# Kernel optimization log

Hardware: AMD Instinct MI355X
Metric: run time of the kernel (lower is better)

The kernel has to match this reference:

```python
import jax, jax.numpy as jnp
import numpy as np
import math

B, L, E, H = 512, 200, 64, 4
D = E // H
NEG = jnp.float32(-(2.0 ** 32) + 1.0)


def setup_inputs() -> dict:
    key = jax.random.key(0)
    ks = jax.random.split(key, 12)
    inp = jax.random.normal(ks[0], (B, L, E), dtype=jnp.float32)
    # realistic variable-length histories: mask[b, t] = t < len_b, len_b in [1, L]
    lens = jax.random.randint(ks[1], (B, 1), 1, L + 1)
    mask = jnp.arange(L)[None, :] < lens  # [B, L] bool
    s = 1.0 / math.sqrt(E)
    pos_enc = jax.random.normal(ks[2], (1, L, E), dtype=jnp.float32)
    Wk = jax.random.uniform(ks[3], (E, E), jnp.float32, -s, s)
    bk = jnp.zeros((E,), jnp.float32)
    Wv = jax.random.uniform(ks[4], (E, E), jnp.float32, -s, s)
    bv = jnp.zeros((E,), jnp.float32)
    Wq = jax.random.uniform(ks[5], (E, E), jnp.float32, -s, s)
    bq = jnp.zeros((E,), jnp.float32)
    Wf = jax.random.uniform(ks[6], (E, E), jnp.float32, -s, s)
    bf = jnp.zeros((E,), jnp.float32)
    return {"input": inp, "mask": mask, "pos_enc": pos_enc,
            "Wk": Wk, "bk": bk, "Wv": Wv, "bv": bv,
            "Wq": Wq, "bq": bq, "Wf": Wf, "bf": bf}


def reference(input, mask, pos_enc, Wk, bk, Wv, bv, Wq, bq, Wf, bf):
    x = input + pos_enc  # [B, L, E]
    # project and split heads: [B, H, L, D]
    def split(t):
        return t.reshape(B, L, H, D).transpose(0, 2, 1, 3)
    k = split(x @ Wk.T + bk)
    v = split(x @ Wv.T + bv)
    q = split(x @ Wq.T + bq) / math.sqrt(D)
    scores = jnp.einsum('bhqd,bhkd->bhqk', q, k)  # [B, H, L, L]
    # key_mask in torch code broadcasts over dim 3 (mask on the QUERY axis),
    # query_mask is its transpose (mask on the KEY axis). Combined: both must be valid.
    both = mask[:, None, :, None] & mask[:, None, None, :]  # [B, 1, L, L]
    scores = jnp.where(both, scores, NEG)
    attn = jax.nn.softmax(scores, axis=-1)
    # dropout is identity at inference; omitted deterministically
    out = jnp.einsum('bhqk,bhkd->bhqd', attn, v)
    out = out.transpose(0, 2, 1, 3).reshape(B, L, E)
    out = out @ Wf.T + bf
    fm = mask.astype(jnp.float32)[:, :, None]  # [B, L, 1]
    lens = jnp.sum(fm, axis=1)  # [B, 1]
    pooled = jnp.sum(out * fm, axis=1) / (lens + 1e-8)  # [B, E]
    return pooled
```

## Files before the change

kernel.cpp:

```cpp
#include <hip/hip_runtime.h>
#include <hip/hip_fp16.h>
#include <math.h>

#define Bn 512
#define Ln 200
#define En 64
#define Hn 4
#define Dn 16
#define NT13 13
#define RMAX 208
#define XS 72
#define KS 36
#define VS 212

typedef _Float16 __f16;
typedef __f16 f16x4 __attribute__((ext_vector_type(4)));
typedef __f16 f16x8 __attribute__((ext_vector_type(8)));
typedef float f32x4 __attribute__((ext_vector_type(4)));

__device__ __forceinline__ f16x8 pack8(float4 a, float4 b) {
    f16x8 r;
    r[0] = (__f16)a.x; r[1] = (__f16)a.y; r[2] = (__f16)a.z; r[3] = (__f16)a.w;
    r[4] = (__f16)b.x; r[5] = (__f16)b.y; r[6] = (__f16)b.z; r[7] = (__f16)b.w;
    return r;
}

__global__ __launch_bounds__(256, 3) void fused_kernel(
    const float* __restrict__ input, const int* __restrict__ mask,
    const float* __restrict__ pos_enc,
    const float* __restrict__ Wk, const float* __restrict__ bk,
    const float* __restrict__ Wv, const float* __restrict__ bv,
    const float* __restrict__ Wq, const float* __restrict__ bq,
    float* __restrict__ pooled)
{
    __shared__ __align__(16) __f16 xw[4][16 * XS];
    __shared__ __align__(16) __f16 Kh[RMAX * KS];
    __shared__ __align__(16) __f16 Qh[RMAX * KS];
    __shared__ __align__(16) __f16 Vt[32 * VS];
    __shared__ float red[4][16];
    __shared__ int cnt_red[4];

    const int tid  = threadIdx.x;
    const int b    = blockIdx.x >> 1, hp = blockIdx.x & 1;
    const int wave = tid >> 6, lane = tid & 63;
    const int quad = lane >> 4, ln16 = lane & 15;

    const int mv = (tid < Ln) ? mask[b * Ln + tid] : 0;

    f16x8 bfr[3][2][2];
    #pragma unroll
    for (int m = 0; m < 3; ++m) {
        const float* W = (m == 0) ? Wk : (m == 1) ? Wv : Wq;
        #pragma unroll
        for (int ct = 0; ct < 2; ++ct)
            #pragma unroll
            for (int ks = 0; ks < 2; ++ks) {
                const float4* wp = (const float4*)(W + (size_t)(hp * 32 + ct * 16 + ln16) * 64) + (ks * 8 + quad * 2);
                bfr[m][ct][ks] = pack8(wp[0], wp[1]);
            }
    }
    float bkv[2], bvv[2], bqv[2];
    #pragma unroll
    for (int ct = 0; ct < 2; ++ct) {
        int cg = hp * 32 + ct * 16 + ln16;
        bkv[ct] = bk[cg]; bvv[ct] = bv[cg]; bqv[ct] = bq[cg];
    }

    const float4* in4 = (const float4*)(input + (size_t)b * Ln * En);
    const float4* pe4 = (const float4*)pos_enc;
    __f16* myx = xw[wave];

    for (int rt = wave; rt < NT13; rt += 4) {
        #pragma unroll
        for (int i = 0; i < 4; ++i) {
            const int gi = lane + (i << 6);
            const int r = gi >> 4, c4 = gi & 15;
            const int R = rt * 16 + r;
            float4 xv = {0,0,0,0}, pv = {0,0,0,0};
            if (R < Ln) { xv = in4[R * 16 + c4]; pv = pe4[R * 16 + c4]; }
            f16x4 hx;
            hx[0] = (__f16)(xv.x + pv.x); hx[1] = (__f16)(xv.y + pv.y);
            hx[2] = (__f16)(xv.z + pv.z); hx[3] = (__f16)(xv.w + pv.w);
            *(f16x4*)(myx + r * XS + c4 * 4) = hx;
        }

        f16x8 af[2];
        #pragma unroll
        for (int ks = 0; ks < 2; ++ks)
            af[ks] = *(const f16x8*)(myx + ln16 * XS + ks * 32 + quad * 8);

        f32x4 acc[3][2];
        #pragma unroll
        for (int m = 0; m < 3; ++m)
            #pragma unroll
            for (int ct = 0; ct < 2; ++ct)
                acc[m][ct] = (f32x4){0.f, 0.f, 0.f, 0.f};
        #pragma unroll
        for (int ks = 0; ks < 2; ++ks)
            #pragma unroll
            for (int m = 0; m < 3; ++m)
                #pragma unroll
                for (int ct = 0; ct < 2; ++ct)
                    acc[m][ct] = __builtin_amdgcn_mfma_f32_16x16x32_f16(af[ks], bfr[m][ct][ks], acc[m][ct], 0, 0, 0);

        #pragma unroll
        for (int ct = 0; ct < 2; ++ct) {
            #pragma unroll
            for (int j = 0; j < 4; ++j) {
                int t = rt * 16 + quad * 4 + j;
                Kh[t * KS + ct * 16 + ln16] = (__f16)(acc[0][ct][j] + bkv[ct]);
                Qh[t * KS + ct * 16 + ln16] = (__f16)((acc[2][ct][j] + bqv[ct]) * 0.25f);
            }
            f16x4 vp;
            #pragma unroll
            for (int j = 0; j < 4; ++j) vp[j] = (__f16)(acc[1][ct][j] + bvv[ct]);
            *(f16x4*)(Vt + (ct * 16 + ln16) * VS + rt * 16 + quad * 4) = vp;
        }
    }

    int c = (mv != 0) ? 1 : 0;
    #pragma unroll
    for (int off = 32; off; off >>= 1) c += __shfl_down(c, off, 64);
    if (lane == 0) cnt_red[wave] = c;
    __syncthreads();
    const int len = cnt_red[0] + cnt_red[1] + cnt_red[2] + cnt_red[3];
    const int nt  = (len + 15) >> 4;

    const int hl   = wave >> 1;
    const int hoff = hl * 16;
    const int npair = (nt + 1) >> 1;
    f32x4 pool = {0.f, 0.f, 0.f, 0.f};

    for (int p = (wave & 1); p < npair; p += 2) {
        const int qt0 = 2 * p, qt1 = 2 * p + 1;
        const int qr1 = min(qt1 * 16 + ln16, RMAX - 1);
        const f16x4 qf0 = *(const f16x4*)(Qh + (qt0 * 16 + ln16) * KS + hoff + quad * 4);
        const f16x4 qf1 = *(const f16x4*)(Qh + qr1 * KS + hoff + quad * 4);
        f32x4 o20 = {0,0,0,0}, o21 = {0,0,0,0};
        float l0 = 0.f, l1 = 0.f;

        for (int kt = 0; kt < nt - 1; ++kt) {
            const f16x4 kf = *(const f16x4*)(Kh + (kt * 16 + ln16) * KS + hoff + quad * 4);
            const f16x4 vf = *(const f16x4*)(Vt + (hoff + ln16) * VS + kt * 16 + quad * 4);
            f32x4 s0 = __builtin_amdgcn_mfma_f32_16x16x16f16(kf, qf0, (f32x4){0,0,0,0}, 0, 0, 0);
            f32x4 s1 = __builtin_amdgcn_mfma_f32_16x16x16f16(kf, qf1, (f32x4){0,0,0,0}, 0, 0, 0);
            f16x4 pf0, pf1;
            #pragma unroll
            for (int j = 0; j < 4; ++j) {
                float p0 = __expf(fminf(s0[j], 10.f));
                float p1 = __expf(fminf(s1[j], 10.f));
                l0 += p0; l1 += p1;
                pf0[j] = (__f16)p0; pf1[j] = (__f16)p1;
            }
            o20 = __builtin_amdgcn_mfma_f32_16x16x16f16(vf, pf0, o20, 0, 0, 0);
            o21 = __builtin_amdgcn_mfma_f32_16x16x16f16(vf, pf1, o21, 0, 0, 0);
        }
        {
            const int kt = nt - 1;
            const int kbase = kt * 16 + quad * 4;
            const f16x4 kf = *(const f16x4*)(Kh + (kt * 16 + ln16) * KS + hoff + quad * 4);
            const f16x4 vf = *(const f16x4*)(Vt + (hoff + ln16) * VS + kt * 16 + quad * 4);
            f32x4 s0 = __builtin_amdgcn_mfma_f32_16x16x16f16(kf, qf0, (f32x4){0,0,0,0}, 0, 0, 0);
            f32x4 s1 = __builtin_amdgcn_mfma_f32_16x16x16f16(kf, qf1, (f32x4){0,0,0,0}, 0, 0, 0);
            f16x4 pf0, pf1;
            #pragma unroll
            for (int j = 0; j < 4; ++j) {
                const bool kok = (kbase + j) < len;
                float p0 = kok ? __expf(fminf(s0[j], 10.f)) : 0.f;
                float p1 = kok ? __expf(fminf(s1[j], 10.f)) : 0.f;
                l0 += p0; l1 += p1;
                pf0[j] = (__f16)p0; pf1[j] = (__f16)p1;
            }
            o20 = __builtin_amdgcn_mfma_f32_16x16x16f16(vf, pf0, o20, 0, 0, 0);
            o21 = __builtin_amdgcn_mfma_f32_16x16x16f16(vf, pf1, o21, 0, 0, 0);
        }

        l0 += __shfl_xor(l0, 16, 64); l0 += __shfl_xor(l0, 32, 64);
        l1 += __shfl_xor(l1, 16, 64); l1 += __shfl_xor(l1, 32, 64);
        const float rs0 = (qt0 * 16 + ln16 < len) ? 1.f / l0 : 0.f;
        const float rs1 = (qt1 * 16 + ln16 < len) ? 1.f / l1 : 0.f;
        #pragma unroll
        for (int j = 0; j < 4; ++j)
            pool[j] = fmaf(o20[j], rs0, fmaf(o21[j], rs1, pool[j]));
    }

    #pragma unroll
    for (int j = 0; j < 4; ++j) {
        #pragma unroll
        for (int off = 1; off < 16; off <<= 1) pool[j] += __shfl_xor(pool[j], off, 64);
    }
    if (ln16 == 0) {
        #pragma unroll
        for (int j = 0; j < 4; ++j) red[wave][quad * 4 + j] = pool[j];
    }
    __syncthreads();
    if (tid < 32) {
        int hl2 = tid >> 4, vd = tid & 15;
        float sres = red[hl2 * 2][vd] + red[hl2 * 2 + 1][vd];
        pooled[b * En + hp * 32 + hl2 * 16 + vd] = sres / ((float)len + 1e-8f);
    }
}

__global__ __launch_bounds__(256) void final_kernel(
    const float* __restrict__ pooled, const float* __restrict__ Wf,
    const float* __restrict__ bf_, float* __restrict__ out)
{
    __shared__ float Wfs[En * 65];
    __shared__ float accs[4][En];
    const int tid = threadIdx.x, wave = tid >> 6, lane = tid & 63;
    const int b = blockIdx.x * 4 + wave;

    const float4* Wf4 = (const float4*)Wf;
    for (int idx4 = tid; idx4 < En * 16; idx4 += 256) {
        int e = idx4 >> 4, i4 = idx4 & 15;
        float4 w = Wf4[idx4];
        Wfs[e * 65 + i4 * 4 + 0] = w.x;
        Wfs[e * 65 + i4 * 4 + 1] = w.y;
        Wfs[e * 65 + i4 * 4 + 2] = w.z;
        Wfs[e * 65 + i4 * 4 + 3] = w.w;
    }
    accs[wave][lane] = pooled[b * En + lane];
    __syncthreads();

    float s = 0.f;
    #pragma unroll
    for (int i = 0; i < En; ++i)
        s = fmaf(accs[wave][i], Wfs[lane * 65 + i], s);
    out[b * En + lane] = s + bf_[lane];
}

extern "C" void kernel_launch(void* const* d_in, const int* in_sizes, int n_in,
                              void* d_out, int out_size, void* d_ws, size_t ws_size,
                              hipStream_t stream) {
    const float* input   = (const float*)d_in[0];
    const int*   mask    = (const int*)  d_in[1];
    const float* pos_enc = (const float*)d_in[2];
    const float* Wk      = (const float*)d_in[3];
    const float* bk      = (const float*)d_in[4];
    const float* Wv      = (const float*)d_in[5];
    const float* bv      = (const float*)d_in[6];
    const float* Wq      = (const float*)d_in[7];
    const float* bq      = (const float*)d_in[8];
    const float* Wf      = (const float*)d_in[9];
    const float* bf      = (const float*)d_in[10];

    float* pooled = (float*)d_ws;
    float* out    = (float*)d_out;

    fused_kernel<<<Bn * 2, 256, 0, stream>>>(input, mask, pos_enc,
                                             Wk, bk, Wv, bv, Wq, bq, pooled);
    final_kernel<<<Bn / 4, 256, 0, stream>>>(pooled, Wf, bf, out);
}
```

Measured before the change: 126.6 us.

## Fuse output projection via atomics, process four query tiles per pass, use exp2

Removes the separate final projection kernel: each block multiplies its half of the pooled vector by the matching columns of Wf and atomically adds into the output, which is zeroed by a memset first. The attention loop now handles four query tiles per pass instead of two and software-prefetches the next K/V fragments, so each K/V load is reused across more MFMAs. Softmax switches to a native exp2 with log2(e) folded into the Q scale. The atomics make the output order-dependent in float rounding, and the extra per-pass registers may lower occupancy.

```diff
diff --git a/kernel.cpp b/kernel.cpp
--- a/kernel.cpp
+++ b/kernel.cpp
@@ -12,11 +12,18 @@
 #define XS 72
 #define KS 36
 #define VS 212
+#define QSC 0.36067376022224085f
 
 typedef _Float16 __f16;
 typedef __f16 f16x4 __attribute__((ext_vector_type(4)));
 typedef __f16 f16x8 __attribute__((ext_vector_type(8)));
 typedef float f32x4 __attribute__((ext_vector_type(4)));
+
+#if __has_builtin(__builtin_amdgcn_exp2f)
+__device__ __forceinline__ float fexp2(float x) { return __builtin_amdgcn_exp2f(x); }
+#else
+__device__ __forceinline__ float fexp2(float x) { return exp2f(x); }
+#endif
 
 __device__ __forceinline__ f16x8 pack8(float4 a, float4 b) {
     f16x8 r;
@@ -31,13 +38,15 @@
     const float* __restrict__ Wk, const float* __restrict__ bk,
     const float* __restrict__ Wv, const float* __restrict__ bv,
     const float* __restrict__ Wq, const float* __restrict__ bq,
-    float* __restrict__ pooled)
+    const float* __restrict__ Wf, const float* __restrict__ bf_,
+    float* __restrict__ out)
 {
     __shared__ __align__(16) __f16 xw[4][16 * XS];
     __shared__ __align__(16) __f16 Kh[RMAX * KS];
     __shared__ __align__(16) __f16 Qh[RMAX * KS];
     __shared__ __align__(16) __f16 Vt[32 * VS];
     __shared__ float red[4][16];
+    __shared__ float ph[32];
     __shared__ int cnt_red[4];
 
     const int tid  = threadIdx.x;
@@ -45,7 +54,8 @@
     const int wave = tid >> 6, lane = tid & 63;
     const int quad = lane >> 4, ln16 = lane & 15;
 
-    const int mv = (tid < Ln) ? mask[b * Ln + tid] : 0;
+    int c = 0;
+    for (int t = tid; t < Ln; t += 256) c += (mask[b * Ln + t] != 0) ? 1 : 0;
 
     f16x8 bfr[3][2][2];
     #pragma unroll
@@ -93,8 +103,7 @@
         #pragma unroll
         for (int m = 0; m < 3; ++m)
             #pragma unroll
-            for (int ct = 0; ct < 2; ++ct)
-                acc[m][ct] = (f32x4){0.f, 0.f, 0.f, 0.f};
+            for (int ct = 0; ct < 2; ++ct) acc[m][ct] = (f32x4){0,0,0,0};
         #pragma unroll
         for (int ks = 0; ks < 2; ++ks)
             #pragma unroll
@@ -109,7 +118,7 @@
             for (int j = 0; j < 4; ++j) {
                 int t = rt * 16 + quad * 4 + j;
                 Kh[t * KS + ct * 16 + ln16] = (__f16)(acc[0][ct][j] + bkv[ct]);
-                Qh[t * KS + ct * 16 + ln16] = (__f16)((acc[2][ct][j] + bqv[ct]) * 0.25f);
+                Qh[t * KS + ct * 16 + ln16] = (__f16)((acc[2][ct][j] + bqv[ct]) * QSC);
             }
             f16x4 vp;
             #pragma unroll
@@ -118,70 +127,86 @@
         }
     }
 
-    int c = (mv != 0) ? 1 : 0;
     #pragma unroll
     for (int off = 32; off; off >>= 1) c += __shfl_down(c, off, 64);
     if (lane == 0) cnt_red[wave] = c;
     __syncthreads();
     const int len = cnt_red[0] + cnt_red[1] + cnt_red[2] + cnt_red[3];
-    const int nt  = (len + 15) >> 4;
-
-    const int hl   = wave >> 1;
+    const int nt = (len + 15) >> 4;
+
+    const int hl = wave >> 1;
     const int hoff = hl * 16;
-    const int npair = (nt + 1) >> 1;
+    const int nquad = (nt + 3) >> 2;
     f32x4 pool = {0.f, 0.f, 0.f, 0.f};
 
-    for (int p = (wave & 1); p < npair; p += 2) {
-        const int qt0 = 2 * p, qt1 = 2 * p + 1;
-        const int qr1 = min(qt1 * 16 + ln16, RMAX - 1);
-        const f16x4 qf0 = *(const f16x4*)(Qh + (qt0 * 16 + ln16) * KS + hoff + quad * 4);
-        const f16x4 qf1 = *(const f16x4*)(Qh + qr1 * KS + hoff + quad * 4);
-        f32x4 o20 = {0,0,0,0}, o21 = {0,0,0,0};
-        float l0 = 0.f, l1 = 0.f;
+    for (int g = (wave & 1); g < nquad; g += 2) {
+        const int qt0 = 4 * g;
+        f16x4 qf[4];
+        #pragma unroll
+        for (int i = 0; i < 4; ++i) {
+            int qr = min((qt0 + i) * 16 + ln16, RMAX - 1);
+            qf[i] = *(const f16x4*)(Qh + qr * KS + hoff + quad * 4);
+        }
+        f32x4 o2[4];
+        float l[4] = {0.f, 0.f, 0.f, 0.f};
+        #pragma unroll
+        for (int i = 0; i < 4; ++i) o2[i] = (f32x4){0,0,0,0};
+
+        f16x4 kf = *(const f16x4*)(Kh + ln16 * KS + hoff + quad * 4);
+        f16x4 vf = *(const f16x4*)(Vt + (hoff + ln16) * VS + quad * 4);
 
         for (int kt = 0; kt < nt - 1; ++kt) {
-            const f16x4 kf = *(const f16x4*)(Kh + (kt * 16 + ln16) * KS + hoff + quad * 4);
-            const f16x4 vf = *(const f16x4*)(Vt + (hoff + ln16) * VS + kt * 16 + quad * 4);
-            f32x4 s0 = __builtin_amdgcn_mfma_f32_16x16x16f16(kf, qf0, (f32x4){0,0,0,0}, 0, 0, 0);
-            f32x4 s1 = __builtin_amdgcn_mfma_f32_16x16x16f16(kf, qf1, (f32x4){0,0,0,0}, 0, 0, 0);
-            f16x4 pf0, pf1;
-            #pragma unroll
-            for (int j = 0; j < 4; ++j) {
-                float p0 = __expf(fminf(s0[j], 10.f));
-                float p1 = __expf(fminf(s1[j], 10.f));
-                l0 += p0; l1 += p1;
-                pf0[j] = (__f16)p0; pf1[j] = (__f16)p1;
-            }
-            o20 = __builtin_amdgcn_mfma_f32_16x16x16f16(vf, pf0, o20, 0, 0, 0);
-            o21 = __builtin_amdgcn_mfma_f32_16x16x16f16(vf, pf1, o21, 0, 0, 0);
+            const f16x4 kfn = *(const f16x4*)(Kh + ((kt + 1) * 16 + ln16) * KS + hoff + quad * 4);
+            const f16x4 vfn = *(const f16x4*)(Vt + (hoff + ln16) * VS + (kt + 1) * 16 + quad * 4);
+            f32x4 s[4];
+            #pragma unroll
+            for (int i = 0; i < 4; ++i)
+                s[i] = __builtin_amdgcn_mfma_f32_16x16x16f16(kf, qf[i], (f32x4){0,0,0,0}, 0, 0, 0);
+            f16x4 pf[4];
+            #pragma unroll
+            for (int i = 0; i < 4; ++i) {
+                #pragma unroll
+                for (int j = 0; j < 4; ++j) {
+                    float p = fexp2(fminf(s[i][j], 14.5f));
+                    l[i] += p;
+                    pf[i][j] = (__f16)p;
+                }
+            }
+            #pragma unroll
+            for (int i = 0; i < 4; ++i)
+                o2[i] = __builtin_amdgcn_mfma_f32_16x16x16f16(vf, pf[i], o2[i], 0, 0, 0);
+            kf = kfn; vf = vfn;
         }
         {
-            const int kt = nt - 1;
-            const int kbase = kt * 16 + quad * 4;
-            const f16x4 kf = *(const f16x4*)(Kh + (kt * 16 + ln16) * KS + hoff + quad * 4);
-            const f16x4 vf = *(const f16x4*)(Vt + (hoff + ln16) * VS + kt * 16 + quad * 4);
-            f32x4 s0 = __builtin_amdgcn_mfma_f32_16x16x16f16(kf, qf0, (f32x4){0,0,0,0}, 0, 0, 0);
-            f32x4 s1 = __builtin_amdgcn_mfma_f32_16x16x16f16(kf, qf1, (f32x4){0,0,0,0}, 0, 0, 0);
-            f16x4 pf0, pf1;
-            #pragma unroll
-            for (int j = 0; j < 4; ++j) {
-                const bool kok = (kbase + j) < len;
-                float p0 = kok ? __expf(fminf(s0[j], 10.f)) : 0.f;
-                float p1 = kok ? __expf(fminf(s1[j], 10.f)) : 0.f;
-                l0 += p0; l1 += p1;
-                pf0[j] = (__f16)p0; pf1[j] = (__f16)p1;
-            }
-            o20 = __builtin_amdgcn_mfma_f32_16x16x16f16(vf, pf0, o20, 0, 0, 0);
-            o21 = __builtin_amdgcn_mfma_f32_16x16x16f16(vf, pf1, o21, 0, 0, 0);
-        }
-
-        l0 += __shfl_xor(l0, 16, 64); l0 += __shfl_xor(l0, 32, 64);
-        l1 += __shfl_xor(l1, 16, 64); l1 += __shfl_xor(l1, 32, 64);
-        const float rs0 = (qt0 * 16 + ln16 < len) ? 1.f / l0 : 0.f;
-        const float rs1 = (qt1 * 16 + ln16 < len) ? 1.f / l1 : 0.f;
-        #pragma unroll
-        for (int j = 0; j < 4; ++j)
-            pool[j] = fmaf(o20[j], rs0, fmaf(o21[j], rs1, pool[j]));
+            const int kbase = (nt - 1) * 16 + quad * 4;
+            f32x4 s[4];
+            #pragma unroll
+            for (int i = 0; i < 4; ++i)
+                s[i] = __builtin_amdgcn_mfma_f32_16x16x16f16(kf, qf[i], (f32x4){0,0,0,0}, 0, 0, 0);
+            f16x4 pf[4];
+            #pragma unroll
+            for (int i = 0; i < 4; ++i) {
+                #pragma unroll
+                for (int j = 0; j < 4; ++j) {
+                    const bool kok = (kbase + j) < len;
+                    float p = kok ? fexp2(fminf(s[i][j], 14.5f)) : 0.f;
+                    l[i] += p;
+                    pf[i][j] = (__f16)p;
+                }
+            }
+            #pragma unroll
+            for (int i = 0; i < 4; ++i)
+                o2[i] = __builtin_amdgcn_mfma_f32_16x16x16f16(vf, pf[i], o2[i], 0, 0, 0);
+        }
+
+        #pragma unroll
+        for (int i = 0; i < 4; ++i) {
+            l[i] += __shfl_xor(l[i], 16, 64);
+            l[i] += __shfl_xor(l[i], 32, 64);
+            const float rs = ((qt0 + i) * 16 + ln16 < len) ? 1.f / l[i] : 0.f;
+            #pragma unroll
+            for (int j = 0; j < 4; ++j) pool[j] = fmaf(o2[i][j], rs, pool[j]);
+        }
     }
 
     #pragma unroll
@@ -197,36 +222,18 @@
     if (tid < 32) {
         int hl2 = tid >> 4, vd = tid & 15;
         float sres = red[hl2 * 2][vd] + red[hl2 * 2 + 1][vd];
-        pooled[b * En + hp * 32 + hl2 * 16 + vd] = sres / ((float)len + 1e-8f);
-    }
-}
-
-__global__ __launch_bounds__(256) void final_kernel(
-    const float* __restrict__ pooled, const float* __restrict__ Wf,
-    const float* __restrict__ bf_, float* __restrict__ out)
-{
-    __shared__ float Wfs[En * 65];
-    __shared__ float accs[4][En];
-    const int tid = threadIdx.x, wave = tid >> 6, lane = tid & 63;
-    const int b = blockIdx.x * 4 + wave;
-
-    const float4* Wf4 = (const float4*)Wf;
-    for (int idx4 = tid; idx4 < En * 16; idx4 += 256) {
-        int e = idx4 >> 4, i4 = idx4 & 15;
-        float4 w = Wf4[idx4];
-        Wfs[e * 65 + i4 * 4 + 0] = w.x;
-        Wfs[e * 65 + i4 * 4 + 1] = w.y;
-        Wfs[e * 65 + i4 * 4 + 2] = w.z;
-        Wfs[e * 65 + i4 * 4 + 3] = w.w;
-    }
-    accs[wave][lane] = pooled[b * En + lane];
+        ph[tid] = sres / ((float)len + 1e-8f);
+    }
     __syncthreads();
 
-    float s = 0.f;
-    #pragma unroll
-    for (int i = 0; i < En; ++i)
-        s = fmaf(accs[wave][i], Wfs[lane * 65 + i], s);
-    out[b * En + lane] = s + bf_[lane];
+    if (tid < 64) {
+        const int e = tid;
+        const float* wr = Wf + (size_t)e * 64 + hp * 32;
+        float a = (hp == 0) ? bf_[e] : 0.f;
+        #pragma unroll
+        for (int i = 0; i < 32; ++i) a = fmaf(wr[i], ph[i], a);
+        atomicAdd(out + b * En + e, a);
+    }
 }
 
 extern "C" void kernel_launch(void* const* d_in, const int* in_sizes, int n_in,
@@ -244,10 +251,9 @@
     const float* Wf      = (const float*)d_in[9];
     const float* bf      = (const float*)d_in[10];
 
-    float* pooled = (float*)d_ws;
-    float* out    = (float*)d_out;
+    float* out = (float*)d_out;
+    hipMemsetAsync(out, 0, (size_t)Bn * En * sizeof(float), stream);
 
     fused_kernel<<<Bn * 2, 256, 0, stream>>>(input, mask, pos_enc,
-                                             Wk, bk, Wv, bv, Wq, bq, pooled);
-    final_kernel<<<Bn / 4, 256, 0, stream>>>(pooled, Wf, bf, out);
+                                             Wk, bk, Wv, bv, Wq, bq, Wf, bf, out);
 }
```

Result: no change. 125.8 us (-0.6%).
